# Kernel tuning notes

Measured on AMD Instinct MI355X. Metric: run time of the kernel, lower is better.

## Reference

```python
import jax, jax.numpy as jnp
import numpy as np

B = 16384
IN = 512
H = 512

def setup_inputs() -> dict:
    key = jax.random.key(0)
    ks = jax.random.split(key, 8)
    inp = {
        "x_t": jax.random.normal(ks[0], (B, IN), dtype=jnp.float32),
        "h_t": jax.random.normal(ks[1], (B, H), dtype=jnp.float32),
        "W_ir": jax.random.normal(ks[2], (IN, H), dtype=jnp.float32),
        "W_hr": jax.random.normal(ks[3], (H, H), dtype=jnp.float32),
        "b_r": jnp.zeros((H,), dtype=jnp.float32),
        "W_iz": jax.random.normal(ks[4], (IN, H), dtype=jnp.float32),
        "W_hz": jax.random.normal(ks[5], (H, H), dtype=jnp.float32),
        "b_z": jnp.zeros((H,), dtype=jnp.float32),
        "W_in": jax.random.normal(ks[6], (IN, H), dtype=jnp.float32),
        "W_hn": jax.random.normal(ks[7], (H, H), dtype=jnp.float32),
        "b_n": jnp.zeros((H,), dtype=jnp.float32),
    }
    return inp

def reference(x_t, h_t, W_ir, W_hr, b_r, W_iz, W_hz, b_z, W_in, W_hn, b_n):
    # Fuse the three input-side and three hidden-side GEMMs by concatenating weights.
    Wi = jnp.concatenate([W_ir, W_iz, W_in], axis=1)   # [IN, 3H]
    Wh = jnp.concatenate([W_hr, W_hz, W_hn], axis=1)   # [H, 3H]
    gi = x_t @ Wi                                      # [B, 3H]
    gh = h_t @ Wh                                      # [B, 3H]
    h = b_r.shape[0]
    r_t = jax.nn.sigmoid(gi[:, :h] + gh[:, :h] + b_r)
    z_t = jax.nn.sigmoid(gi[:, h:2*h] + gh[:, h:2*h] + b_z)
    n_t = jnp.tanh(gi[:, 2*h:] + r_t * gh[:, 2*h:] + b_n)
    return (1.0 - z_t) * n_t + z_t * h_t
```

## Files before the change

kernel.cpp:

```cpp
#include <hip/hip_runtime.h>
#include <hip/hip_fp16.h>

typedef _Float16 half8 __attribute__((ext_vector_type(8)));
typedef float floatx4 __attribute__((ext_vector_type(4)));

#define AS1 __attribute__((address_space(1)))
#define AS3 __attribute__((address_space(3)))

#define WLO_OFF (6 * 512 * 512)
#define WMAT_STRIDE ((size_t)(8 * 16 * 2048))
#define APERM_OFF ((size_t)(2 * WLO_OFF))
#define APERM_HALFS ((size_t)128 * 16 * 4 * 4096)

__device__ __forceinline__ void async_lds16(const void* g, void* l) {
  __builtin_amdgcn_global_load_lds((const AS1 void*)g, (AS3 void*)l, 16, 0, 0);
}

__global__ __launch_bounds__(256) void prep(
    const float* __restrict__ x, const float* __restrict__ h,
    const float* __restrict__ Wir, const float* __restrict__ Whr,
    const float* __restrict__ Wiz, const float* __restrict__ Whz,
    const float* __restrict__ Win, const float* __restrict__ Whn,
    _Float16* __restrict__ wperm) {
  __shared__ __align__(16) float xt[128 * 68];
  __shared__ __align__(16) float ht[128 * 68];
  const int b = blockIdx.x;
  const int t = threadIdx.x;

  if (b >= 1024) {
    const int b2 = b - 1024;
    const int w = b2 >> 7;
    const int rem = b2 & 127;
    const int ki = rem >> 3;
    const int nt = rem & 7;
    const float* W = (w == 0) ? Wir : (w == 1) ? Whr : (w == 2) ? Wiz
                   : (w == 3) ? Whz : (w == 4) ? Win : Whn;
    const int k0 = ki * 32, n0 = nt * 64;
    const int kk = t >> 3;
    const int nn = (t & 7) * 8;
    const float* src = W + (k0 + kk) * 512 + n0 + nn;
    float4 f0 = *(const float4*)(src);
    float4 f1 = *(const float4*)(src + 4);
    float* drow = xt + kk * 68 + nn;
    *(float4*)(drow) = f0;
    *(float4*)(drow + 4) = f1;
    __syncthreads();
    const int u = t >> 6, l = t & 63;
    const int nloc = 16 * u + (l & 15);
    const int kbase = 8 * (l >> 4);
    half8 vh2, vl2;
#pragma unroll
    for (int j = 0; j < 8; ++j) {
      float f = xt[(kbase + j) * 68 + nloc];
      _Float16 hi = (_Float16)f;
      _Float16 lo = (_Float16)(f - (float)hi);
      vh2[j] = hi;
      vl2[j] = lo;
    }
    const size_t off = ((size_t)((w * 8 + nt) * 16 + ki)) * 2048 + t * 8;
    *(half8*)(wperm + off) = vh2;
    *(half8*)(wperm + WLO_OFF + off) = vl2;
    return;
  }

  const int mt = b >> 3;
  const int kp = b & 7;
#pragma unroll
  for (int p = 0; p < 2; ++p) {
    const int r = (t >> 2) + p * 64;
    const int c = (t & 3) * 16;
    const float* sx = x + ((size_t)(mt * 128 + r)) * 512 + kp * 64 + c;
    const float* sh = h + ((size_t)(mt * 128 + r)) * 512 + kp * 64 + c;
    float4 a0 = *(const float4*)(sx);
    float4 a1 = *(const float4*)(sx + 4);
    float4 a2 = *(const float4*)(sx + 8);
    float4 a3 = *(const float4*)(sx + 12);
    float4 b0 = *(const float4*)(sh);
    float4 b1 = *(const float4*)(sh + 4);
    float4 b2 = *(const float4*)(sh + 8);
    float4 b3 = *(const float4*)(sh + 12);
    float* dx = xt + r * 68 + c;
    float* dh = ht + r * 68 + c;
    *(float4*)(dx) = a0; *(float4*)(dx + 4) = a1;
    *(float4*)(dx + 8) = a2; *(float4*)(dx + 12) = a3;
    *(float4*)(dh) = b0; *(float4*)(dh + 4) = b1;
    *(float4*)(dh + 8) = b2; *(float4*)(dh + 12) = b3;
  }
  __syncthreads();

#pragma unroll
  for (int ii = 0; ii < 2; ++ii) {
    const int kt = kp * 2 + ii;
    const int cb = ii * 32;
    _Float16* dst = wperm + APERM_OFF + ((size_t)(mt * 16 + kt)) * 16384;
#pragma unroll
    for (int hc = 0; hc < 2; ++hc) {
      const int cc = t + hc * 256;
      const int m = 16 * (cc >> 6) + (cc & 15);
      const int kA = 8 * ((cc >> 4) & 3);
      half8 xh, xl, hh, hl;
#pragma unroll
      for (int j = 0; j < 8; ++j) {
        float fx = xt[m * 68 + cb + kA + j];
        float fh = ht[m * 68 + cb + kA + j];
        _Float16 a = (_Float16)fx;
        xh[j] = a; xl[j] = (_Float16)(fx - (float)a);
        _Float16 bb = (_Float16)fh;
        hh[j] = bb; hl[j] = (_Float16)(fh - (float)bb);
      }
      *(half8*)(dst + 0 * 4096 + cc * 8) = xh;
      *(half8*)(dst + 1 * 4096 + cc * 8) = xl;
      *(half8*)(dst + 2 * 4096 + cc * 8) = hh;
      *(half8*)(dst + 3 * 4096 + cc * 8) = hl;
    }
  }
}

__global__ __launch_bounds__(256, 2) void gru_fused2(
    const float* __restrict__ h, const _Float16* __restrict__ wperm,
    const float* __restrict__ br, const float* __restrict__ bz,
    const float* __restrict__ bn, float* __restrict__ out) {
  __shared__ __align__(16) _Float16 ldsA[2 * 4 * 4096];

  const int t = threadIdx.x;
  const int lane = t & 63;
  const int wv = t >> 6;
  const int bid = blockIdx.x;
  const int xcd = bid & 7;
  const int g = bid >> 3;
  const int nt = g & 7;
  const int mt = (g >> 3) * 8 + xcd;
  const int m0 = mt * 128;
  const int n0 = nt * 64;
  const _Float16* wlo = wperm + WLO_OFF;
  const _Float16* aperm = wperm + APERM_OFF + (size_t)mt * 16 * 16384;

  floatx4 acc_r[8] = {};
  floatx4 acc_z[8] = {};
  floatx4 acc_in[8] = {};
  floatx4 acc_hn[8] = {};

  {
    const _Float16* asrc = aperm + wv * 4096 + lane * 8;
    _Float16* adst = ldsA + wv * 4096;
#pragma unroll
    for (int q = 0; q < 8; ++q) async_lds16(asrc + q * 512, adst + q * 512);
  }
  __syncthreads();

#pragma unroll 2
  for (int kt = 0; kt < 16; ++kt) {
    const _Float16* A = ldsA + (kt & 1) * 16384;

    const size_t tb = ((size_t)(nt * 16 + kt)) * 2048 + wv * 512 + lane * 8;
    half8 bh_ir = *(const half8*)(wperm + tb + 0 * WMAT_STRIDE);
    half8 bh_hr = *(const half8*)(wperm + tb + 1 * WMAT_STRIDE);
    half8 bh_iz = *(const half8*)(wperm + tb + 2 * WMAT_STRIDE);
    half8 bh_hz = *(const half8*)(wperm + tb + 3 * WMAT_STRIDE);
    half8 bh_in = *(const half8*)(wperm + tb + 4 * WMAT_STRIDE);
    half8 bh_hn = *(const half8*)(wperm + tb + 5 * WMAT_STRIDE);
    half8 bl_ir = *(const half8*)(wlo + tb + 0 * WMAT_STRIDE);
    half8 bl_hr = *(const half8*)(wlo + tb + 1 * WMAT_STRIDE);
    half8 bl_iz = *(const half8*)(wlo + tb + 2 * WMAT_STRIDE);
    half8 bl_hz = *(const half8*)(wlo + tb + 3 * WMAT_STRIDE);
    half8 bl_in = *(const half8*)(wlo + tb + 4 * WMAT_STRIDE);
    half8 bl_hn = *(const half8*)(wlo + tb + 5 * WMAT_STRIDE);
    __builtin_amdgcn_sched_barrier(0);

    if (kt < 15) {
      const _Float16* asrc =
          aperm + (size_t)(kt + 1) * 16384 + wv * 4096 + lane * 8;
      _Float16* adst = ldsA + ((kt & 1) ^ 1) * 16384 + wv * 4096;
#pragma unroll
      for (int q = 0; q < 8; ++q) async_lds16(asrc + q * 512, adst + q * 512);
    }
    __builtin_amdgcn_sched_barrier(0);

    __builtin_amdgcn_s_setprio(1);
#pragma unroll
    for (int i = 0; i < 8; ++i) {
      const int ao = (i * 64 + lane) * 8;
      half8 axh = *(const half8*)(A + 0 * 4096 + ao);
      half8 axl = *(const half8*)(A + 1 * 4096 + ao);
      half8 ahh = *(const half8*)(A + 2 * 4096 + ao);
      half8 ahl = *(const half8*)(A + 3 * 4096 + ao);
      acc_r[i]  = __builtin_amdgcn_mfma_f32_16x16x32_f16(axh, bh_ir, acc_r[i], 0, 0, 0);
      acc_r[i]  = __builtin_amdgcn_mfma_f32_16x16x32_f16(ahh, bh_hr, acc_r[i], 0, 0, 0);
      acc_z[i]  = __builtin_amdgcn_mfma_f32_16x16x32_f16(axh, bh_iz, acc_z[i], 0, 0, 0);
      acc_z[i]  = __builtin_amdgcn_mfma_f32_16x16x32_f16(ahh, bh_hz, acc_z[i], 0, 0, 0);
      acc_in[i] = __builtin_amdgcn_mfma_f32_16x16x32_f16(axh, bh_in, acc_in[i], 0, 0, 0);
      acc_hn[i] = __builtin_amdgcn_mfma_f32_16x16x32_f16(ahh, bh_hn, acc_hn[i], 0, 0, 0);
      acc_r[i]  = __builtin_amdgcn_mfma_f32_16x16x32_f16(axl, bh_ir, acc_r[i], 0, 0, 0);
      acc_r[i]  = __builtin_amdgcn_mfma_f32_16x16x32_f16(ahl, bh_hr, acc_r[i], 0, 0, 0);
      acc_z[i]  = __builtin_amdgcn_mfma_f32_16x16x32_f16(axl, bh_iz, acc_z[i], 0, 0, 0);
      acc_z[i]  = __builtin_amdgcn_mfma_f32_16x16x32_f16(ahl, bh_hz, acc_z[i], 0, 0, 0);
      acc_in[i] = __builtin_amdgcn_mfma_f32_16x16x32_f16(axl, bh_in, acc_in[i], 0, 0, 0);
      acc_hn[i] = __builtin_amdgcn_mfma_f32_16x16x32_f16(ahl, bh_hn, acc_hn[i], 0, 0, 0);
      acc_r[i]  = __builtin_amdgcn_mfma_f32_16x16x32_f16(axh, bl_ir, acc_r[i], 0, 0, 0);
      acc_r[i]  = __builtin_amdgcn_mfma_f32_16x16x32_f16(ahh, bl_hr, acc_r[i], 0, 0, 0);
      acc_z[i]  = __builtin_amdgcn_mfma_f32_16x16x32_f16(axh, bl_iz, acc_z[i], 0, 0, 0);
      acc_z[i]  = __builtin_amdgcn_mfma_f32_16x16x32_f16(ahh, bl_hz, acc_z[i], 0, 0, 0);
      acc_in[i] = __builtin_amdgcn_mfma_f32_16x16x32_f16(axh, bl_in, acc_in[i], 0, 0, 0);
      acc_hn[i] = __builtin_amdgcn_mfma_f32_16x16x32_f16(ahh, bl_hn, acc_hn[i], 0, 0, 0);
    }
    __builtin_amdgcn_s_setprio(0);

    __syncthreads();
  }

  const int quad = lane >> 4;
  const int col = lane & 15;
  const int n = n0 + wv * 16 + col;
  const float vbr = br[n], vbz = bz[n], vbn = bn[n];
#pragma unroll
  for (int i = 0; i < 8; ++i) {
    const int mbase = m0 + i * 16 + quad * 4;
#pragma unroll
    for (int r = 0; r < 4; ++r) {
      const int m = mbase + r;
      const float gr = acc_r[i][r] + vbr;
      const float gz = acc_z[i][r] + vbz;
      const float rg = 1.0f / (1.0f + __expf(-gr));
      const float zg = 1.0f / (1.0f + __expf(-gz));
      const float gn = acc_in[i][r] + rg * acc_hn[i][r] + vbn;
      const float e2 = __expf(2.0f * gn);
      const float ntv = 1.0f - 2.0f / (e2 + 1.0f);
      const float hp = h[m * 512 + n];
      out[m * 512 + n] = (1.0f - zg) * ntv + zg * hp;
    }
  }
}

__global__ __launch_bounds__(256) void permute_w_old(
    const float* __restrict__ Wir, const float* __restrict__ Whr,
    const float* __restrict__ Wiz, const float* __restrict__ Whz,
    const float* __restrict__ Win, const float* __restrict__ Whn,
    _Float16* __restrict__ wperm) {
  __shared__ __align__(16) float tile[32 * 68];
  const int b = blockIdx.x;
  const int t = threadIdx.x;
  const int w = b >> 7;
  const int rem = b & 127;
  const int ki = rem >> 3;
  const int nt = rem & 7;
  const float* W = (w == 0) ? Wir : (w == 1) ? Whr : (w == 2) ? Wiz
                 : (w == 3) ? Whz : (w == 4) ? Win : Whn;
  const int k0 = ki * 32, n0 = nt * 64;
  const int kk = t >> 3;
  const int nn = (t & 7) * 8;
  const float* src = W + (k0 + kk) * 512 + n0 + nn;
  float4 f0 = *(const float4*)(src);
  float4 f1 = *(const float4*)(src + 4);
  float* drow = tile + kk * 68 + nn;
  *(float4*)(drow) = f0;
  *(float4*)(drow + 4) = f1;
  __syncthreads();
  const int u = t >> 6, l = t & 63;
  const int nloc = 16 * u + (l & 15);
  const int kbase = 8 * (l >> 4);
  half8 vh2, vl2;
#pragma unroll
  for (int j = 0; j < 8; ++j) {
    float f = tile[(kbase + j) * 68 + nloc];
    _Float16 hi = (_Float16)f;
    _Float16 lo = (_Float16)(f - (float)hi);
    vh2[j] = hi;
    vl2[j] = lo;
  }
  const size_t off = ((size_t)((w * 8 + nt) * 16 + ki)) * 2048 + t * 8;
  *(half8*)(wperm + off) = vh2;
  *(half8*)(wperm + WLO_OFF + off) = vl2;
}

__global__ __launch_bounds__(256, 2) void gru_fused_fb(
    const float* __restrict__ x, const float* __restrict__ h,
    const _Float16* __restrict__ wperm,
    const float* __restrict__ br, const float* __restrict__ bz,
    const float* __restrict__ bn, float* __restrict__ out) {
  __shared__ __align__(16) _Float16 ldsA[2 * 4 * 4096];
  const int t = threadIdx.x;
  const int lane = t & 63;
  const int wn = t >> 6;
  const int bid = blockIdx.x;
  const int nt = bid & 7;
  const int mt = bid >> 3;
  const int m0 = mt * 128;
  const int n0 = nt * 64;
  const _Float16* wlo = wperm + WLO_OFF;

  floatx4 acc_r[8] = {};
  floatx4 acc_z[8] = {};
  floatx4 acc_in[8] = {};
  floatx4 acc_hn[8] = {};

  const int mA = 16 * (t >> 6) + (t & 15);
  const int kA = 8 * ((t >> 4) & 3);
  const float* px0 = x + (m0 + mA) * 512 + kA;
  const float* ph0 = h + (m0 + mA) * 512 + kA;
  const float* px1 = px0 + 64 * 512;
  const float* ph1 = ph0 + 64 * 512;
  const int c0 = t, c1 = t + 256;

  {
    float v[4][8];
    *(float4*)&v[0][0] = *(const float4*)(px0); *(float4*)&v[0][4] = *(const float4*)(px0 + 4);
    *(float4*)&v[1][0] = *(const float4*)(px1); *(float4*)&v[1][4] = *(const float4*)(px1 + 4);
    *(float4*)&v[2][0] = *(const float4*)(ph0); *(float4*)&v[2][4] = *(const float4*)(ph0 + 4);
    *(float4*)&v[3][0] = *(const float4*)(ph1); *(float4*)&v[3][4] = *(const float4*)(ph1 + 4);
#pragma unroll
    for (int g = 0; g < 4; ++g) {
      half8 hi, lo;
#pragma unroll
      for (int j = 0; j < 8; ++j) {
        _Float16 a = (_Float16)v[g][j];
        hi[j] = a;
        lo[j] = (_Float16)(v[g][j] - (float)a);
      }
      const int c = (g & 1) ? c1 : c0;
      const int part = (g >> 1) * 2;
      *(half8*)(ldsA + (part + 0) * 4096 + c * 8) = hi;
      *(half8*)(ldsA + (part + 1) * 4096 + c * 8) = lo;
    }
  }
  __syncthreads();

#pragma unroll 2
  for (int kt = 0; kt < 16; ++kt) {
    const _Float16* A = ldsA + (kt & 1) * 16384;
    const size_t tb = ((size_t)(nt * 16 + kt)) * 2048 + wn * 512 + lane * 8;
    half8 bh_ir = *(const half8*)(wperm + tb + 0 * WMAT_STRIDE);
    half8 bh_hr = *(const half8*)(wperm + tb + 1 * WMAT_STRIDE);
    half8 bh_iz = *(const half8*)(wperm + tb + 2 * WMAT_STRIDE);
    half8 bh_hz = *(const half8*)(wperm + tb + 3 * WMAT_STRIDE);
    half8 bh_in = *(const half8*)(wperm + tb + 4 * WMAT_STRIDE);
    half8 bh_hn = *(const half8*)(wperm + tb + 5 * WMAT_STRIDE);
    half8 bl_ir = *(const half8*)(wlo + tb + 0 * WMAT_STRIDE);
    half8 bl_hr = *(const half8*)(wlo + tb + 1 * WMAT_STRIDE);
    half8 bl_iz = *(const half8*)(wlo + tb + 2 * WMAT_STRIDE);
    half8 bl_hz = *(const half8*)(wlo + tb + 3 * WMAT_STRIDE);
    half8 bl_in = *(const half8*)(wlo + tb + 4 * WMAT_STRIDE);
    half8 bl_hn = *(const half8*)(wlo + tb + 5 * WMAT_STRIDE);
    __builtin_amdgcn_sched_barrier(0);

    float v[4][8];
    if (kt < 15) {
      const int k0 = (kt + 1) * 32;
      *(float4*)&v[0][0] = *(const float4*)(px0 + k0); *(float4*)&v[0][4] = *(const float4*)(px0 + k0 + 4);
      *(float4*)&v[1][0] = *(const float4*)(px1 + k0); *(float4*)&v[1][4] = *(const float4*)(px1 + k0 + 4);
      *(float4*)&v[2][0] = *(const float4*)(ph0 + k0); *(float4*)&v[2][4] = *(const float4*)(ph0 + k0 + 4);
      *(float4*)&v[3][0] = *(const float4*)(ph1 + k0); *(float4*)&v[3][4] = *(const float4*)(ph1 + k0 + 4);
    }
    __builtin_amdgcn_sched_barrier(0);

    __builtin_amdgcn_s_setprio(1);
#pragma unroll
    for (int i = 0; i < 8; ++i) {
      const int ao = (i * 64 + lane) * 8;
      half8 axh = *(const half8*)(A + 0 * 4096 + ao);
      half8 axl = *(const half8*)(A + 1 * 4096 + ao);
      half8 ahh = *(const half8*)(A + 2 * 4096 + ao);
      half8 ahl = *(const half8*)(A + 3 * 4096 + ao);
      acc_r[i]  = __builtin_amdgcn_mfma_f32_16x16x32_f16(axh, bh_ir, acc_r[i], 0, 0, 0);
      acc_r[i]  = __builtin_amdgcn_mfma_f32_16x16x32_f16(ahh, bh_hr, acc_r[i], 0, 0, 0);
      acc_z[i]  = __builtin_amdgcn_mfma_f32_16x16x32_f16(axh, bh_iz, acc_z[i], 0, 0, 0);
      acc_z[i]  = __builtin_amdgcn_mfma_f32_16x16x32_f16(ahh, bh_hz, acc_z[i], 0, 0, 0);
      acc_in[i] = __builtin_amdgcn_mfma_f32_16x16x32_f16(axh, bh_in, acc_in[i], 0, 0, 0);
      acc_hn[i] = __builtin_amdgcn_mfma_f32_16x16x32_f16(ahh, bh_hn, acc_hn[i], 0, 0, 0);
      acc_r[i]  = __builtin_amdgcn_mfma_f32_16x16x32_f16(axl, bh_ir, acc_r[i], 0, 0, 0);
      acc_r[i]  = __builtin_amdgcn_mfma_f32_16x16x32_f16(ahl, bh_hr, acc_r[i], 0, 0, 0);
      acc_z[i]  = __builtin_amdgcn_mfma_f32_16x16x32_f16(axl, bh_iz, acc_z[i], 0, 0, 0);
      acc_z[i]  = __builtin_amdgcn_mfma_f32_16x16x32_f16(ahl, bh_hz, acc_z[i], 0, 0, 0);
      acc_in[i] = __builtin_amdgcn_mfma_f32_16x16x32_f16(axl, bh_in, acc_in[i], 0, 0, 0);
      acc_hn[i] = __builtin_amdgcn_mfma_f32_16x16x32_f16(ahl, bh_hn, acc_hn[i], 0, 0, 0);
      acc_r[i]  = __builtin_amdgcn_mfma_f32_16x16x32_f16(axh, bl_ir, acc_r[i], 0, 0, 0);
      acc_r[i]  = __builtin_amdgcn_mfma_f32_16x16x32_f16(ahh, bl_hr, acc_r[i], 0, 0, 0);
      acc_z[i]  = __builtin_amdgcn_mfma_f32_16x16x32_f16(axh, bl_iz, acc_z[i], 0, 0, 0);
      acc_z[i]  = __builtin_amdgcn_mfma_f32_16x16x32_f16(ahh, bl_hz, acc_z[i], 0, 0, 0);
      acc_in[i] = __builtin_amdgcn_mfma_f32_16x16x32_f16(axh, bl_in, acc_in[i], 0, 0, 0);
      acc_hn[i] = __builtin_amdgcn_mfma_f32_16x16x32_f16(ahh, bl_hn, acc_hn[i], 0, 0, 0);
    }
    __builtin_amdgcn_s_setprio(0);

    if (kt < 15) {
      _Float16* base = ldsA + ((kt & 1) ^ 1) * 16384;
#pragma unroll
      for (int g = 0; g < 4; ++g) {
        half8 hi, lo;
#pragma unroll
        for (int j = 0; j < 8; ++j) {
          _Float16 a = (_Float16)v[g][j];
          hi[j] = a;
          lo[j] = (_Float16)(v[g][j] - (float)a);
        }
        const int c = (g & 1) ? c1 : c0;
        const int part = (g >> 1) * 2;
        *(half8*)(base + (part + 0) * 4096 + c * 8) = hi;
        *(half8*)(base + (part + 1) * 4096 + c * 8) = lo;
      }
    }
    __syncthreads();
  }

  const int quad = lane >> 4;
  const int col = lane & 15;
  const int n = n0 + wn * 16 + col;
  const float vbr = br[n], vbz = bz[n], vbn = bn[n];
#pragma unroll
  for (int i = 0; i < 8; ++i) {
    const int mbase = m0 + i * 16 + quad * 4;
#pragma unroll
    for (int r = 0; r < 4; ++r) {
      const int m = mbase + r;
      const float gr = acc_r[i][r] + vbr;
      const float gz = acc_z[i][r] + vbz;
      const float rg = 1.0f / (1.0f + __expf(-gr));
      const float zg = 1.0f / (1.0f + __expf(-gz));
      const float gn = acc_in[i][r] + rg * acc_hn[i][r] + vbn;
      const float e2 = __expf(2.0f * gn);
      const float ntv = 1.0f - 2.0f / (e2 + 1.0f);
      const float hp = h[m * 512 + n];
      out[m * 512 + n] = (1.0f - zg) * ntv + zg * hp;
    }
  }
}

extern "C" void kernel_launch(void* const* d_in, const int* in_sizes, int n_in,
                              void* d_out, int out_size, void* d_ws, size_t ws_size,
                              hipStream_t stream) {
  const float* x   = (const float*)d_in[0];
  const float* h   = (const float*)d_in[1];
  const float* Wir = (const float*)d_in[2];
  const float* Whr = (const float*)d_in[3];
  const float* br  = (const float*)d_in[4];
  const float* Wiz = (const float*)d_in[5];
  const float* Whz = (const float*)d_in[6];
  const float* bz  = (const float*)d_in[7];
  const float* Win = (const float*)d_in[8];
  const float* Whn = (const float*)d_in[9];
  const float* bn  = (const float*)d_in[10];
  float* out = (float*)d_out;
  _Float16* wperm = (_Float16*)d_ws;

  const size_t need_bytes = (APERM_OFF + APERM_HALFS) * 2;
  if (ws_size >= need_bytes) {
    prep<<<1792, 256, 0, stream>>>(x, h, Wir, Whr, Wiz, Whz, Win, Whn, wperm);
    gru_fused2<<<1024, 256, 0, stream>>>(h, wperm, br, bz, bn, out);
  } else {
    permute_w_old<<<768, 256, 0, stream>>>(Wir, Whr, Wiz, Whz, Win, Whn, wperm);
    gru_fused_fb<<<1024, 256, 0, stream>>>(x, h, wperm, br, bz, bn, out);
  }
}
```

Before: 258.5 us.

## Halve prep LDS staging tile and change main kernel block-to-tile mapping

The prep kernel now stages 64 rows of x and h at a time in shared memory instead of 128, looping twice with barriers. This halves the LDS footprint so more blocks can be resident. The GRU kernel drops its XCD-aware block swizzle and maps block id directly to (mt, nt), so the eight n-tiles of one row tile are now spread across different XCDs. That likely hurts L2 reuse of the A panel, and the added barriers in prep cost extra synchronisation.

```diff
diff --git a/kernel.cpp b/kernel.cpp
--- a/kernel.cpp
+++ b/kernel.cpp
@@ -22,8 +22,8 @@
     const float* __restrict__ Wiz, const float* __restrict__ Whz,
     const float* __restrict__ Win, const float* __restrict__ Whn,
     _Float16* __restrict__ wperm) {
-  __shared__ __align__(16) float xt[128 * 68];
-  __shared__ __align__(16) float ht[128 * 68];
+  __shared__ __align__(16) float xt[64 * 68];
+  __shared__ __align__(16) float ht[64 * 68];
   const int b = blockIdx.x;
   const int t = threadIdx.x;
 
@@ -65,44 +65,44 @@
 
   const int mt = b >> 3;
   const int kp = b & 7;
+  _Float16* dstbase = wperm + APERM_OFF + ((size_t)(mt * 16)) * 16384;
+
 #pragma unroll
   for (int p = 0; p < 2; ++p) {
-    const int r = (t >> 2) + p * 64;
-    const int c = (t & 3) * 16;
-    const float* sx = x + ((size_t)(mt * 128 + r)) * 512 + kp * 64 + c;
-    const float* sh = h + ((size_t)(mt * 128 + r)) * 512 + kp * 64 + c;
-    float4 a0 = *(const float4*)(sx);
-    float4 a1 = *(const float4*)(sx + 4);
-    float4 a2 = *(const float4*)(sx + 8);
-    float4 a3 = *(const float4*)(sx + 12);
-    float4 b0 = *(const float4*)(sh);
-    float4 b1 = *(const float4*)(sh + 4);
-    float4 b2 = *(const float4*)(sh + 8);
-    float4 b3 = *(const float4*)(sh + 12);
-    float* dx = xt + r * 68 + c;
-    float* dh = ht + r * 68 + c;
-    *(float4*)(dx) = a0; *(float4*)(dx + 4) = a1;
-    *(float4*)(dx + 8) = a2; *(float4*)(dx + 12) = a3;
-    *(float4*)(dh) = b0; *(float4*)(dh + 4) = b1;
-    *(float4*)(dh + 8) = b2; *(float4*)(dh + 12) = b3;
-  }
-  __syncthreads();
-
-#pragma unroll
-  for (int ii = 0; ii < 2; ++ii) {
-    const int kt = kp * 2 + ii;
-    const int cb = ii * 32;
-    _Float16* dst = wperm + APERM_OFF + ((size_t)(mt * 16 + kt)) * 16384;
-#pragma unroll
-    for (int hc = 0; hc < 2; ++hc) {
-      const int cc = t + hc * 256;
-      const int m = 16 * (cc >> 6) + (cc & 15);
-      const int kA = 8 * ((cc >> 4) & 3);
+    {
+      const int r = t >> 2;
+      const int c = (t & 3) * 16;
+      const float* sx = x + ((size_t)(mt * 128 + 64 * p + r)) * 512 + kp * 64 + c;
+      const float* sh = h + ((size_t)(mt * 128 + 64 * p + r)) * 512 + kp * 64 + c;
+      float4 a0 = *(const float4*)(sx);
+      float4 a1 = *(const float4*)(sx + 4);
+      float4 a2 = *(const float4*)(sx + 8);
+      float4 a3 = *(const float4*)(sx + 12);
+      float4 b0 = *(const float4*)(sh);
+      float4 b1 = *(const float4*)(sh + 4);
+      float4 b2 = *(const float4*)(sh + 8);
+      float4 b3 = *(const float4*)(sh + 12);
+      float* dx = xt + r * 68 + c;
+      float* dh = ht + r * 68 + c;
+      *(float4*)(dx) = a0; *(float4*)(dx + 4) = a1;
+      *(float4*)(dx + 8) = a2; *(float4*)(dx + 12) = a3;
+      *(float4*)(dh) = b0; *(float4*)(dh + 4) = b1;
+      *(float4*)(dh + 8) = b2; *(float4*)(dh + 12) = b3;
+    }
+    __syncthreads();
+
+    const int mloc = 16 * (t >> 6) + (t & 15);
+    const int kA = 8 * ((t >> 4) & 3);
+    const int cc = p * 256 + t;
+#pragma unroll
+    for (int ii = 0; ii < 2; ++ii) {
+      const int cb = ii * 32;
+      _Float16* dst = dstbase + (size_t)(kp * 2 + ii) * 16384;
       half8 xh, xl, hh, hl;
 #pragma unroll
       for (int j = 0; j < 8; ++j) {
-        float fx = xt[m * 68 + cb + kA + j];
-        float fh = ht[m * 68 + cb + kA + j];
+        float fx = xt[mloc * 68 + cb + kA + j];
+        float fh = ht[mloc * 68 + cb + kA + j];
         _Float16 a = (_Float16)fx;
         xh[j] = a; xl[j] = (_Float16)(fx - (float)a);
         _Float16 bb = (_Float16)fh;
@@ -113,6 +113,7 @@
       *(half8*)(dst + 2 * 4096 + cc * 8) = hh;
       *(half8*)(dst + 3 * 4096 + cc * 8) = hl;
     }
+    __syncthreads();
   }
 }
 
@@ -126,10 +127,8 @@
   const int lane = t & 63;
   const int wv = t >> 6;
   const int bid = blockIdx.x;
-  const int xcd = bid & 7;
-  const int g = bid >> 3;
-  const int nt = g & 7;
-  const int mt = (g >> 3) * 8 + xcd;
+  const int nt = bid & 7;
+  const int mt = bid >> 3;
   const int m0 = mt * 128;
   const int n0 = nt * 64;
   const _Float16* wlo = wperm + WLO_OFF;
```

Result: no change. 257.3 us (-0.5%).
